# Optimization experiments

Hardware: AMD Instinct MI355X
Metric: run time of the kernel (lower is better)

## Reference

```python
import jax, jax.numpy as jnp
import numpy as np

EMBED_DIM = 1024
NUM_HEADS = 16
HEAD_DIM = EMBED_DIM // NUM_HEADS
SCALE = HEAD_DIM ** -0.5
B, S = 4, 2048


def setup_inputs() -> dict:
    key = jax.random.key(0)
    ks = jax.random.split(key, 11)
    std = EMBED_DIM ** -0.5
    return {
        "query": jax.random.normal(ks[0], (B, S, EMBED_DIM), jnp.float32),
        "key": jax.random.normal(ks[1], (B, S, EMBED_DIM), jnp.float32),
        "value": jax.random.normal(ks[2], (B, S, EMBED_DIM), jnp.float32),
        "Wq": jax.random.normal(ks[3], (EMBED_DIM, EMBED_DIM), jnp.float32) * std,
        "bq": jax.random.normal(ks[4], (EMBED_DIM,), jnp.float32) * 0.01,
        "Wk": jax.random.normal(ks[5], (EMBED_DIM, EMBED_DIM), jnp.float32) * std,
        "bk": jax.random.normal(ks[6], (EMBED_DIM,), jnp.float32) * 0.01,
        "Wv": jax.random.normal(ks[7], (EMBED_DIM, EMBED_DIM), jnp.float32) * std,
        "bv": jax.random.normal(ks[8], (EMBED_DIM,), jnp.float32) * 0.01,
        "Wo": jax.random.normal(ks[9], (EMBED_DIM, EMBED_DIM), jnp.float32) * std,
        "bo": jax.random.normal(ks[10], (EMBED_DIM,), jnp.float32) * 0.01,
    }


def reference(query, key, value, Wq, bq, Wk, bk, Wv, bv, Wo, bo):
    b, s, _ = query.shape
    # torch.nn.Linear: x @ W.T + b
    q = query @ Wq.T + bq
    k = key @ Wk.T + bk
    v = value @ Wv.T + bv
    # [b, h, s, d]
    q = q.reshape(b, s, NUM_HEADS, HEAD_DIM).transpose(0, 2, 1, 3)
    k = k.reshape(b, s, NUM_HEADS, HEAD_DIM).transpose(0, 2, 1, 3)
    v = v.reshape(b, s, NUM_HEADS, HEAD_DIM).transpose(0, 2, 1, 3)
    # explicit scores [b, h, s, s]
    scores = jnp.einsum("bhqd,bhkd->bhqk", q, k) * SCALE
    causal = jnp.tril(jnp.ones((s, s), dtype=bool))  # is_causal=True
    scores = jnp.where(causal, scores, -jnp.inf)
    attn = jax.nn.softmax(scores, axis=-1)
    out = jnp.einsum("bhqk,bhkd->bhqd", attn, v)
    out = out.transpose(0, 2, 1, 3).reshape(b, s, EMBED_DIM)
    return out @ Wo.T + bo
```

## Files before the change

### kernel.cpp

```cpp
#include <hip/hip_runtime.h>


#define E 1024
#define HEADS 16
#define HD 64
#define SEQ 2048
#define BATCH 4
#define MROWS (BATCH * SEQ)

typedef __bf16 bf16x8 __attribute__((ext_vector_type(8)));
typedef __bf16 bf16x2 __attribute__((ext_vector_type(2)));
typedef float f32x4 __attribute__((ext_vector_type(4)));
typedef unsigned short ushort8v __attribute__((ext_vector_type(8)));

typedef __attribute__((address_space(1))) void gvoid;
typedef __attribute__((address_space(3))) void lvoid;

__device__ __forceinline__ void async16(const void* g, void* l) {
  __builtin_amdgcn_global_load_lds((gvoid*)g, (lvoid*)l, 16, 0, 0);
}

__device__ __forceinline__ unsigned short f2bf(float f) {
  union { float f; unsigned int u; } v;
  v.f = f;
  unsigned int r = v.u + 0x7FFFu + ((v.u >> 16) & 1u);
  return (unsigned short)(r >> 16);
}

__device__ __forceinline__ unsigned packbf(float a, float b) {
  bf16x2 t;
  t[0] = (__bf16)a;
  t[1] = (__bf16)b;
  return __builtin_bit_cast(unsigned, t);
}

__device__ __forceinline__ void store_out(unsigned short* p, float v) { *p = f2bf(v); }
__device__ __forceinline__ void store_out(float* p, float v) { *p = v; }

struct CastArgs {
  const float* src[4];
  unsigned short* dst[4];
  int n;
};

__global__ __launch_bounds__(256) void cast_kernel(CastArgs a) {
  const float* s = a.src[blockIdx.z];
  unsigned short* d = a.dst[blockIdx.z];
  const int n = a.n;
  const int stride = gridDim.x * blockDim.x * 4;
  for (int i = (blockIdx.x * blockDim.x + threadIdx.x) * 4; i < n; i += stride) {
    float4 v = *(const float4*)(s + i);
    ushort4 o;
    o.x = f2bf(v.x); o.y = f2bf(v.y); o.z = f2bf(v.z); o.w = f2bf(v.w);
    *(ushort4*)(d + i) = o;
  }
}

template <typename OutT>
__device__ __forceinline__ void gemm_body(const unsigned short* __restrict__ A,
                                          const unsigned short* __restrict__ W,
                                          const float* __restrict__ bias,
                                          OutT* __restrict__ out, float scale) {
  __shared__ unsigned short At[128 * 64];
  __shared__ unsigned short Wt[128 * 64];
  const int tid = threadIdx.x;
  const int lane = tid & 63;
  const int wv = tid >> 6;
  const int wm = wv & 1, wn = wv >> 1;
  const int li = lane & 15, g = lane >> 4;
  const int m0 = blockIdx.x * 128, n0 = blockIdx.y * 128;
  f32x4 acc[4][4] = {};

  for (int k0 = 0; k0 < E; k0 += 64) {
    __syncthreads();
#pragma unroll
    for (int i = 0; i < 4; ++i) {
      int c = tid + 256 * i;
      int row = c >> 3, slot = c & 7;
      int gc = slot ^ (row & 7);
      async16(A + (size_t)(m0 + row) * E + k0 + gc * 8, &At[c * 8]);
      async16(W + (size_t)(n0 + row) * E + k0 + gc * 8, &Wt[c * 8]);
    }
    asm volatile("s_waitcnt vmcnt(0)" ::: "memory");
    __syncthreads();
#pragma unroll
    for (int kk = 0; kk < 2; ++kk) {
      bf16x8 af[4], bfr[4];
#pragma unroll
      for (int mt = 0; mt < 4; ++mt) {
        int r = wm * 64 + mt * 16 + li;
        int slot = (kk * 4 + g) ^ (r & 7);
        af[mt] = *(const bf16x8*)&At[r * 64 + slot * 8];
      }
#pragma unroll
      for (int nt = 0; nt < 4; ++nt) {
        int r = wn * 64 + nt * 16 + li;
        int slot = (kk * 4 + g) ^ (r & 7);
        bfr[nt] = *(const bf16x8*)&Wt[r * 64 + slot * 8];
      }
#pragma unroll
      for (int mt = 0; mt < 4; ++mt)
#pragma unroll
        for (int nt = 0; nt < 4; ++nt)
          acc[mt][nt] =
              __builtin_amdgcn_mfma_f32_16x16x32_bf16(af[mt], bfr[nt], acc[mt][nt], 0, 0, 0);
    }
  }

#pragma unroll
  for (int nt = 0; nt < 4; ++nt) {
    int col = n0 + wn * 64 + nt * 16 + li;
    float bv = bias[col];
#pragma unroll
    for (int mt = 0; mt < 4; ++mt) {
#pragma unroll
      for (int r = 0; r < 4; ++r) {
        int row = m0 + wm * 64 + mt * 16 + g * 4 + r;
        store_out(&out[(size_t)row * E + col], (acc[mt][nt][r] + bv) * scale);
      }
    }
  }
}

struct QkvArgs {
  const unsigned short* A[3];
  const unsigned short* W[3];
  const float* bias[3];
  unsigned short* out[3];
  float scale[3];
};

__global__ __launch_bounds__(256) void gemm_qkv(QkvArgs p) {
  const int z = blockIdx.z;
  gemm_body<unsigned short>(p.A[z], p.W[z], p.bias[z], p.out[z], p.scale[z]);
}

__global__ __launch_bounds__(256) void gemm_out_k(const unsigned short* __restrict__ A,
                                                  const unsigned short* __restrict__ W,
                                                  const float* __restrict__ bias,
                                                  float* __restrict__ out) {
  gemm_body<float>(A, W, bias, out, 1.0f);
}

__global__ __launch_bounds__(512, 4) void flash_kernel(const unsigned short* __restrict__ Qb,
                                                       const unsigned short* __restrict__ Kb,
                                                       const unsigned short* __restrict__ Vb,
                                                       unsigned short* __restrict__ Ob) {
  __shared__ unsigned short Kt[2][128 * 64];
  __shared__ unsigned short Vt[2][64 * 128];
  const int p = blockIdx.x;
  const int bh = blockIdx.y;
  const int b = bh >> 4, h16 = bh & 15;
  const size_t base = (size_t)b * SEQ * E + (size_t)h16 * HD;
  const unsigned short* Qp = Qb + base;
  const unsigned short* Kp = Kb + base;
  const unsigned short* Vp = Vb + base;
  unsigned short* Op = Ob + base;
  const int tid = threadIdx.x, lane = tid & 63, wv = tid >> 6;
  const int li = lane & 15, g = lane >> 4;
  const int qlo = p, qhi = 15 - p;
  const int slo = ((g & 1) << 5) | li;

  bf16x8 qfL[2], qfH[2];
#pragma unroll
  for (int kk = 0; kk < 2; ++kk) {
    int rl = qlo * 128 + wv * 16 + li;
    int rh = qhi * 128 + wv * 16 + li;
    qfL[kk] = *(const bf16x8*)(Qp + (size_t)rl * E + kk * 32 + g * 8);
    qfH[kk] = *(const bf16x8*)(Qp + (size_t)rh * E + kk * 32 + g * 8);
  }

  f32x4 oaL[4] = {}, oaH[4] = {};
  float miL = -1e30f, lsL = 0.0f;
  float miH = -1e30f, lsH = 0.0f;

  ushort8v vv[2];

  auto loadV = [&](int j) {
#pragma unroll
    for (int i = 0; i < 2; ++i) {
      int c = tid + 512 * i;
      int key = c & 127, db = (c >> 7) * 8;
      vv[i] = *(const ushort8v*)(Vp + (size_t)(j * 128 + key) * E + db);
    }
  };
  auto stageK = [&](int j, int buf) {
#pragma unroll
    for (int i = 0; i < 2; ++i) {
      int c = tid + 512 * i;
      int row = c >> 3, slot = c & 7;
      int gc = slot ^ (row & 7);
      async16(Kp + (size_t)(j * 128 + row) * E + gc * 8, &Kt[buf][c * 8]);
    }
  };
  auto scatV = [&](int buf) {
#pragma unroll
    for (int i = 0; i < 2; ++i) {
      int c = tid + 512 * i;
      int key = c & 127, db = (c >> 7) * 8;
#pragma unroll
      for (int jj = 0; jj < 8; ++jj) {
        int n = db + jj;
        int slot = (key >> 3) ^ (n & 15);
        Vt[buf][n * 128 + slot * 8 + (key & 7)] = vv[i][jj];
      }
    }
  };

  auto compute = [&](const bf16x8 (&qf)[2], float& mi, float& ls,
                     f32x4 (&oa)[4], bool diag, int buf) {
#pragma unroll
    for (int h = 0; h < 2; ++h) {
      if (diag && h * 64 > wv * 16 + 15) continue;

      f32x4 sacc[4] = {};
#pragma unroll
      for (int kk = 0; kk < 2; ++kk) {
        bf16x8 kf[4];
#pragma unroll
        for (int nt = 0; nt < 4; ++nt) {
          int key = h * 64 + nt * 16 + li;
          int slot = (kk * 4 + g) ^ (key & 7);
          kf[nt] = *(const bf16x8*)&Kt[buf][key * 64 + slot * 8];
        }
#pragma unroll
        for (int nt = 0; nt < 4; ++nt)
          sacc[nt] =
              __builtin_amdgcn_mfma_f32_16x16x32_bf16(kf[nt], qf[kk], sacc[nt], 0, 0, 0);
      }

      if (diag && h * 64 + 63 > wv * 16) {
#pragma unroll
        for (int nt = 0; nt < 4; ++nt)
#pragma unroll
          for (int r = 0; r < 4; ++r) {
            int keyg = h * 64 + nt * 16 + g * 4 + r;
            int qg = wv * 16 + li;
            sacc[nt][r] = (keyg > qg) ? -1e30f : sacc[nt][r];
          }
      }

      float mx = sacc[0][0];
#pragma unroll
      for (int nt = 0; nt < 4; ++nt)
#pragma unroll
        for (int r = 0; r < 4; ++r) mx = fmaxf(mx, sacc[nt][r]);
      mx = fmaxf(mx, __shfl_xor(mx, 16));
      mx = fmaxf(mx, __shfl_xor(mx, 32));
      float mnew = fmaxf(mi, mx);
      float alpha = __expf(mi - mnew);
      mi = mnew;

      unsigned pk[4][2];
      float rs = 0.0f;
#pragma unroll
      for (int nt = 0; nt < 4; ++nt) {
        float p0 = __expf(sacc[nt][0] - mi);
        float p1 = __expf(sacc[nt][1] - mi);
        float p2 = __expf(sacc[nt][2] - mi);
        float p3 = __expf(sacc[nt][3] - mi);
        rs += (p0 + p1) + (p2 + p3);
        pk[nt][0] = packbf(p0, p1);
        pk[nt][1] = packbf(p2, p3);
      }
      {
        float s = rs;
        s += __shfl_xor(s, 16);
        s += __shfl_xor(s, 32);
        ls = ls * alpha + s;
#pragma unroll
        for (int dt = 0; dt < 4; ++dt) oa[dt] *= alpha;
      }

#pragma unroll
      for (int kk2 = 0; kk2 < 2; ++kk2) {
        const int kc = h * 2 + kk2;
        bf16x8 vf[4];
#pragma unroll
        for (int dt = 0; dt < 4; ++dt) {
          int d = dt * 16 + li;
          int slot = (kc * 4 + g) ^ (d & 15);
          vf[dt] = *(const bf16x8*)&Vt[buf][d * 128 + slot * 8];
        }
        int a0 = __shfl((int)pk[kk2 * 2][0], slo);
        int a1 = __shfl((int)pk[kk2 * 2][1], slo);
        int a2 = __shfl((int)pk[kk2 * 2][0], slo + 16);
        int a3 = __shfl((int)pk[kk2 * 2][1], slo + 16);
        int c0 = __shfl((int)pk[kk2 * 2 + 1][0], slo);
        int c1 = __shfl((int)pk[kk2 * 2 + 1][1], slo);
        int c2 = __shfl((int)pk[kk2 * 2 + 1][0], slo + 16);
        int c3 = __shfl((int)pk[kk2 * 2 + 1][1], slo + 16);
        bool hi = (g & 2) != 0;
        uint4 bb;
        bb.x = hi ? c0 : a0;
        bb.y = hi ? c1 : a1;
        bb.z = hi ? c2 : a2;
        bb.w = hi ? c3 : a3;
        bf16x8 pf = __builtin_bit_cast(bf16x8, bb);
#pragma unroll
        for (int dt = 0; dt < 4; ++dt)
          oa[dt] =
              __builtin_amdgcn_mfma_f32_16x16x32_bf16(vf[dt], pf, oa[dt], 0, 0, 0);
      }
    }
  };

  loadV(0);
  stageK(0, 0);
  scatV(0);

  for (int j = 0; j <= qhi; ++j) {
    const int buf = j & 1;
    asm volatile("s_waitcnt vmcnt(0)" ::: "memory");
    __syncthreads();
    if (j < qhi) {
      loadV(j + 1);
      stageK(j + 1, buf ^ 1);
    }
    compute(qfH, miH, lsH, oaH, j == qhi, buf);
    if (j <= qlo) compute(qfL, miL, lsL, oaL, j == qlo, buf);
    if (j < qhi) scatV(buf ^ 1);
  }

#pragma unroll
  for (int t = 0; t < 2; ++t) {
    const int qt = t ? qhi : qlo;
    f32x4(&oa)[4] = t ? oaH : oaL;
    float ls = t ? lsH : lsL;
    float inv = 1.0f / ls;
    int row = qt * 128 + wv * 16 + li;
#pragma unroll
    for (int dt = 0; dt < 4; ++dt) {
      ushort4 w;
      w.x = f2bf(oa[dt][0] * inv);
      w.y = f2bf(oa[dt][1] * inv);
      w.z = f2bf(oa[dt][2] * inv);
      w.w = f2bf(oa[dt][3] * inv);
      *(ushort4*)(Op + (size_t)row * E + dt * 16 + g * 4) = w;
    }
  }
}

extern "C" void kernel_launch(void* const* d_in, const int* in_sizes, int n_in,
                              void* d_out, int out_size, void* d_ws, size_t ws_size,
                              hipStream_t stream) {
  const float* q  = (const float*)d_in[0];
  const float* k  = (const float*)d_in[1];
  const float* v  = (const float*)d_in[2];
  const float* Wq = (const float*)d_in[3];
  const float* bq = (const float*)d_in[4];
  const float* Wk = (const float*)d_in[5];
  const float* bk = (const float*)d_in[6];
  const float* Wv = (const float*)d_in[7];
  const float* bv = (const float*)d_in[8];
  const float* Wo = (const float*)d_in[9];
  const float* bo = (const float*)d_in[10];

  unsigned short* Xq  = (unsigned short*)d_ws;
  unsigned short* Xk  = Xq + (size_t)MROWS * E;
  unsigned short* Xv  = Xk + (size_t)MROWS * E;
  unsigned short* Wqb = Xv + (size_t)MROWS * E;
  unsigned short* Wkb = Wqb + (size_t)E * E;
  unsigned short* Wvb = Wkb + (size_t)E * E;
  unsigned short* Wob = Wvb + (size_t)E * E;
  unsigned short* Qb  = Wob + (size_t)E * E;
  unsigned short* Kb  = Qb + (size_t)MROWS * E;
  unsigned short* Vb  = Kb + (size_t)MROWS * E;
  unsigned short* Og  = Xq;

  CastArgs ca;
  ca.src[0] = q; ca.src[1] = k; ca.src[2] = v; ca.src[3] = nullptr;
  ca.dst[0] = Xq; ca.dst[1] = Xk; ca.dst[2] = Xv; ca.dst[3] = nullptr;
  ca.n = MROWS * E;
  cast_kernel<<<dim3(1024, 1, 3), 256, 0, stream>>>(ca);

  CastArgs cw;
  cw.src[0] = Wq; cw.src[1] = Wk; cw.src[2] = Wv; cw.src[3] = Wo;
  cw.dst[0] = Wqb; cw.dst[1] = Wkb; cw.dst[2] = Wvb; cw.dst[3] = Wob;
  cw.n = E * E;
  cast_kernel<<<dim3(256, 1, 4), 256, 0, stream>>>(cw);

  QkvArgs p;
  p.A[0] = Xq;  p.A[1] = Xk;  p.A[2] = Xv;
  p.W[0] = Wqb; p.W[1] = Wkb; p.W[2] = Wvb;
  p.bias[0] = bq; p.bias[1] = bk; p.bias[2] = bv;
  p.out[0] = Qb; p.out[1] = Kb; p.out[2] = Vb;
  p.scale[0] = 0.125f; p.scale[1] = 1.0f; p.scale[2] = 1.0f;
  gemm_qkv<<<dim3(64, 8, 3), 256, 0, stream>>>(p);

  flash_kernel<<<dim3(8, 64), 512, 0, stream>>>(Qb, Kb, Vb, Og);

  gemm_out_k<<<dim3(64, 8), 256, 0, stream>>>(Og, Wob, bo, (float*)d_out);
}
```

Measured before the change: 402.0 us.

## Share K/V fragments across both query tiles and use 16x16x16 MFMA for PV

Merges the two per-query-tile compute passes into one that loads each K and V fragment from LDS once and feeds both the high and low query tiles. The PV product switches to the 16x16x16 bf16 MFMA so the softmax output fragments already sit in the operand layout. This removes the cross-lane shuffles that repacked P and halves the LDS fragment reads when both tiles are active. In exchange, more accumulators and score tiles are live at once, which raises register pressure and could hurt occupancy at the current launch bounds. It also issues twice as many smaller-K MFMAs for PV.

```diff
diff --git a/kernel.cpp b/kernel.cpp
--- a/kernel.cpp
+++ b/kernel.cpp
@@ -9,8 +9,10 @@
 #define MROWS (BATCH * SEQ)
 
 typedef __bf16 bf16x8 __attribute__((ext_vector_type(8)));
+typedef __bf16 bf16x4 __attribute__((ext_vector_type(4)));
 typedef __bf16 bf16x2 __attribute__((ext_vector_type(2)));
 typedef float f32x4 __attribute__((ext_vector_type(4)));
+typedef short short4v __attribute__((ext_vector_type(4)));
 typedef unsigned short ushort8v __attribute__((ext_vector_type(8)));
 
 typedef __attribute__((address_space(1))) void gvoid;
@@ -27,11 +29,9 @@
   return (unsigned short)(r >> 16);
 }
 
-__device__ __forceinline__ unsigned packbf(float a, float b) {
-  bf16x2 t;
-  t[0] = (__bf16)a;
-  t[1] = (__bf16)b;
-  return __builtin_bit_cast(unsigned, t);
+__device__ __forceinline__ f32x4 mfma16(bf16x4 a, bf16x4 b, f32x4 c) {
+  return __builtin_amdgcn_mfma_f32_16x16x16bf16_1k(
+      __builtin_bit_cast(short4v, a), __builtin_bit_cast(short4v, b), c, 0, 0, 0);
 }
 
 __device__ __forceinline__ void store_out(unsigned short* p, float v) { *p = f2bf(v); }
@@ -159,7 +159,6 @@
   const int tid = threadIdx.x, lane = tid & 63, wv = tid >> 6;
   const int li = lane & 15, g = lane >> 4;
   const int qlo = p, qhi = 15 - p;
-  const int slo = ((g & 1) << 5) | li;
 
   bf16x8 qfL[2], qfH[2];
 #pragma unroll
@@ -207,13 +206,58 @@
     }
   };
 
-  auto compute = [&](const bf16x8 (&qf)[2], float& mi, float& ls,
-                     f32x4 (&oa)[4], bool diag, int buf) {
+  auto softmax_pf = [&](f32x4 (&sacc)[4], float& mi, float& ls, f32x4 (&oa)[4],
+                        bool diag, int h, bf16x4 (&pf)[4]) {
+    if (diag && h * 64 + 63 > wv * 16) {
+#pragma unroll
+      for (int nt = 0; nt < 4; ++nt)
+#pragma unroll
+        for (int r = 0; r < 4; ++r) {
+          int keyg = h * 64 + nt * 16 + g * 4 + r;
+          int qg = wv * 16 + li;
+          sacc[nt][r] = (keyg > qg) ? -1e30f : sacc[nt][r];
+        }
+    }
+    float mx = sacc[0][0];
+#pragma unroll
+    for (int nt = 0; nt < 4; ++nt)
+#pragma unroll
+      for (int r = 0; r < 4; ++r) mx = fmaxf(mx, sacc[nt][r]);
+    mx = fmaxf(mx, __shfl_xor(mx, 16));
+    mx = fmaxf(mx, __shfl_xor(mx, 32));
+    float mnew = fmaxf(mi, mx);
+    float alpha = __expf(mi - mnew);
+    mi = mnew;
+
+    float rs = 0.0f;
+#pragma unroll
+    for (int nt = 0; nt < 4; ++nt) {
+      float p0 = __expf(sacc[nt][0] - mi);
+      float p1 = __expf(sacc[nt][1] - mi);
+      float p2 = __expf(sacc[nt][2] - mi);
+      float p3 = __expf(sacc[nt][3] - mi);
+      rs += (p0 + p1) + (p2 + p3);
+      bf16x4 t;
+      t[0] = (__bf16)p0; t[1] = (__bf16)p1; t[2] = (__bf16)p2; t[3] = (__bf16)p3;
+      pf[nt] = t;
+    }
+    float s = rs;
+    s += __shfl_xor(s, 16);
+    s += __shfl_xor(s, 32);
+    ls = ls * alpha + s;
+#pragma unroll
+    for (int dt = 0; dt < 4; ++dt) oa[dt] *= alpha;
+  };
+
+  auto compute2 = [&](bool doLo, bool diagH, bool diagL, int buf) {
 #pragma unroll
     for (int h = 0; h < 2; ++h) {
-      if (diag && h * 64 > wv * 16 + 15) continue;
-
-      f32x4 sacc[4] = {};
+      const bool skipTop = (h * 64 > wv * 16 + 15);
+      const bool aH = !(diagH && skipTop);
+      const bool aL = doLo && !(diagL && skipTop);
+      if (!aH && !aL) continue;
+
+      f32x4 sH[4] = {}, sL[4] = {};
 #pragma unroll
       for (int kk = 0; kk < 2; ++kk) {
         bf16x8 kf[4];
@@ -224,83 +268,32 @@
           kf[nt] = *(const bf16x8*)&Kt[buf][key * 64 + slot * 8];
         }
 #pragma unroll
-        for (int nt = 0; nt < 4; ++nt)
-          sacc[nt] =
-              __builtin_amdgcn_mfma_f32_16x16x32_bf16(kf[nt], qf[kk], sacc[nt], 0, 0, 0);
-      }
-
-      if (diag && h * 64 + 63 > wv * 16) {
-#pragma unroll
-        for (int nt = 0; nt < 4; ++nt)
-#pragma unroll
-          for (int r = 0; r < 4; ++r) {
-            int keyg = h * 64 + nt * 16 + g * 4 + r;
-            int qg = wv * 16 + li;
-            sacc[nt][r] = (keyg > qg) ? -1e30f : sacc[nt][r];
-          }
-      }
-
-      float mx = sacc[0][0];
-#pragma unroll
-      for (int nt = 0; nt < 4; ++nt)
-#pragma unroll
-        for (int r = 0; r < 4; ++r) mx = fmaxf(mx, sacc[nt][r]);
-      mx = fmaxf(mx, __shfl_xor(mx, 16));
-      mx = fmaxf(mx, __shfl_xor(mx, 32));
-      float mnew = fmaxf(mi, mx);
-      float alpha = __expf(mi - mnew);
-      mi = mnew;
-
-      unsigned pk[4][2];
-      float rs = 0.0f;
-#pragma unroll
-      for (int nt = 0; nt < 4; ++nt) {
-        float p0 = __expf(sacc[nt][0] - mi);
-        float p1 = __expf(sacc[nt][1] - mi);
-        float p2 = __expf(sacc[nt][2] - mi);
-        float p3 = __expf(sacc[nt][3] - mi);
-        rs += (p0 + p1) + (p2 + p3);
-        pk[nt][0] = packbf(p0, p1);
-        pk[nt][1] = packbf(p2, p3);
-      }
-      {
-        float s = rs;
-        s += __shfl_xor(s, 16);
-        s += __shfl_xor(s, 32);
-        ls = ls * alpha + s;
-#pragma unroll
-        for (int dt = 0; dt < 4; ++dt) oa[dt] *= alpha;
-      }
-
-#pragma unroll
-      for (int kk2 = 0; kk2 < 2; ++kk2) {
-        const int kc = h * 2 + kk2;
-        bf16x8 vf[4];
-#pragma unroll
-        for (int dt = 0; dt < 4; ++dt) {
-          int d = dt * 16 + li;
-          int slot = (kc * 4 + g) ^ (d & 15);
-          vf[dt] = *(const bf16x8*)&Vt[buf][d * 128 + slot * 8];
-        }
-        int a0 = __shfl((int)pk[kk2 * 2][0], slo);
-        int a1 = __shfl((int)pk[kk2 * 2][1], slo);
-        int a2 = __shfl((int)pk[kk2 * 2][0], slo + 16);
-        int a3 = __shfl((int)pk[kk2 * 2][1], slo + 16);
-        int c0 = __shfl((int)pk[kk2 * 2 + 1][0], slo);
-        int c1 = __shfl((int)pk[kk2 * 2 + 1][1], slo);
-        int c2 = __shfl((int)pk[kk2 * 2 + 1][0], slo + 16);
-        int c3 = __shfl((int)pk[kk2 * 2 + 1][1], slo + 16);
-        bool hi = (g & 2) != 0;
-        uint4 bb;
-        bb.x = hi ? c0 : a0;
-        bb.y = hi ? c1 : a1;
-        bb.z = hi ? c2 : a2;
-        bb.w = hi ? c3 : a3;
-        bf16x8 pf = __builtin_bit_cast(bf16x8, bb);
-#pragma unroll
-        for (int dt = 0; dt < 4; ++dt)
-          oa[dt] =
-              __builtin_amdgcn_mfma_f32_16x16x32_bf16(vf[dt], pf, oa[dt], 0, 0, 0);
+        for (int nt = 0; nt < 4; ++nt) {
+          if (aH)
+            sH[nt] = __builtin_amdgcn_mfma_f32_16x16x32_bf16(kf[nt], qfH[kk], sH[nt], 0, 0, 0);
+          if (aL)
+            sL[nt] = __builtin_amdgcn_mfma_f32_16x16x32_bf16(kf[nt], qfL[kk], sL[nt], 0, 0, 0);
+        }
+      }
+
+      bf16x4 pfH[4], pfL[4];
+      if (aH) softmax_pf(sH, miH, lsH, oaH, diagH, h, pfH);
+      if (aL) softmax_pf(sL, miL, lsL, oaL, diagL, h, pfL);
+
+#pragma unroll
+      for (int dt = 0; dt < 4; ++dt) {
+        bf16x4 vf[4];
+#pragma unroll
+        for (int c4 = 0; c4 < 4; ++c4) {
+          int c = h * 4 + c4;
+          int slot = (c * 2 + (g >> 1)) ^ li;
+          vf[c4] = *(const bf16x4*)&Vt[buf][(dt * 16 + li) * 128 + slot * 8 + (g & 1) * 4];
+        }
+#pragma unroll
+        for (int c4 = 0; c4 < 4; ++c4) {
+          if (aH) oaH[dt] = mfma16(vf[c4], pfH[c4], oaH[dt]);
+          if (aL) oaL[dt] = mfma16(vf[c4], pfL[c4], oaL[dt]);
+        }
       }
     }
   };
@@ -317,8 +310,7 @@
       loadV(j + 1);
       stageK(j + 1, buf ^ 1);
     }
-    compute(qfH, miH, lsH, oaH, j == qhi, buf);
-    if (j <= qlo) compute(qfL, miL, lsL, oaL, j == qlo, buf);
+    compute2(j <= qlo, j == qhi, j == qlo, buf);
     if (j < qhi) scatV(buf ^ 1);
   }
 
```

Measured after the change: 480.8 us. 19.6% more time.
